# Optimization experiments

Measured on AMD Instinct MI355X. Metric: run time of the kernel, lower is better.

Reference implementation:

```python
import jax, jax.numpy as jnp
import numpy as np

N = 50000
E = 800000
IN_DIM = 128
HID_DIM = 128
OUT_DIM = 128
EPS = 1e-5


def setup_inputs() -> dict:
    key = jax.random.key(0)
    ks = jax.random.split(key, 6)
    x = jax.random.normal(ks[0], (N, IN_DIM), dtype=jnp.float32)
    src = jax.random.randint(ks[1], (E,), 0, N, dtype=jnp.int32)
    dst = jax.random.randint(ks[2], (E,), 0, N, dtype=jnp.int32)
    W1 = jax.random.normal(ks[3], (IN_DIM, HID_DIM), dtype=jnp.float32) / np.sqrt(IN_DIM)
    W2 = jax.random.normal(ks[4], (HID_DIM, OUT_DIM), dtype=jnp.float32) / np.sqrt(HID_DIM)
    return {
        "x": x, "src": src, "dst": dst,
        "W1": W1, "b1": jnp.zeros((HID_DIM,), jnp.float32),
        "gamma1": jnp.ones((HID_DIM,), jnp.float32), "beta1": jnp.zeros((HID_DIM,), jnp.float32),
        "W2": W2, "b2": jnp.zeros((OUT_DIM,), jnp.float32),
        "gamma2": jnp.ones((OUT_DIM,), jnp.float32), "beta2": jnp.zeros((OUT_DIM,), jnp.float32),
    }


def _degrees(src, dst, n):
    ones = jnp.ones(src.shape[0], jnp.float32)
    out_deg = jax.ops.segment_sum(ones, src, num_segments=n)
    in_deg = jax.ops.segment_sum(ones, dst, num_segments=n)
    # DGL norm='both' clamps degree to min 1 before pow(-0.5)
    return jnp.clip(out_deg, 1.0) ** -0.5, jnp.clip(in_deg, 1.0) ** -0.5


def _gconv(h, src, dst, d_out, d_in, W, b):
    h = h * d_out[:, None]                                   # [N, d] src-side norm
    m = jax.ops.segment_sum(h[src], dst, num_segments=h.shape[0])  # SpMM aggregate
    m = m * d_in[:, None]                                    # dst-side norm
    return m @ W + b


def _bn(h, gamma, beta):
    mu = jnp.mean(h, axis=0)
    var = jnp.var(h, axis=0)  # biased, matches torch BN training forward
    return gamma * (h - mu) * jax.lax.rsqrt(var + EPS) + beta


def reference(x, src, dst, W1, b1, gamma1, beta1, W2, b2, gamma2, beta2):
    d_out, d_in = _degrees(src, dst, x.shape[0])
    h1 = jax.nn.relu(_bn(_gconv(x, src, dst, d_out, d_in, W1, b1), gamma1, beta1))
    # dropout is identity in eval mode
    h2 = _bn(_gconv(h1, src, dst, d_out, d_in, W2, b2), gamma2, beta2)
    return jax.nn.relu(h2 + h1)
```

## Files before the change

### kernel.cpp

```cpp
#include <hip/hip_runtime.h>
#include <hip/hip_fp16.h>

#define NODES 50000
#define EDGES 800000
#define DIM 128
#define EPS_BN 1e-5f
#define SCAN_B 1024
#define SCAN_NB ((NODES + SCAN_B - 1) / SCAN_B)
#define GEMM_NB ((NODES + 63) / 64)
#define NCH 64
#define CHE (EDGES / NCH)
#define NR 4
#define RNG (NODES / NR)

typedef _Float16 half8 __attribute__((ext_vector_type(8)));
typedef float floatx4 __attribute__((ext_vector_type(4)));

union H8 { half8 v; __half2 h2[4]; };

__global__ __launch_bounds__(256) void hist_part_kernel(const int* __restrict__ src,
                                                        const int* __restrict__ dst,
                                                        unsigned short* __restrict__ Psrc,
                                                        unsigned short* __restrict__ Pdst) {
    __shared__ int h[RNG];
    int chunk = blockIdx.x & (NCH - 1);
    int range = blockIdx.x >> 6;
    const int* arr = blockIdx.y ? dst : src;
    unsigned short* P = blockIdx.y ? Pdst : Psrc;
    int base = range * RNG;
    for (int i = threadIdx.x; i < RNG; i += 256) h[i] = 0;
    __syncthreads();
    int e0 = chunk * CHE;
    for (int e = e0 + threadIdx.x; e < e0 + CHE; e += 256) {
        unsigned r = (unsigned)(arr[e] - base);
        if (r < (unsigned)RNG) atomicAdd(&h[r], 1);
    }
    __syncthreads();
    for (int i = threadIdx.x; i < RNG; i += 256)
        P[(size_t)chunk * NODES + base + i] = (unsigned short)h[i];
}

__global__ __launch_bounds__(256) void combine_kernel(const unsigned short* __restrict__ Psrc,
                                                      unsigned short* __restrict__ Pdst,
                                                      int* __restrict__ cnt_in,
                                                      float* __restrict__ dn_out,
                                                      float* __restrict__ dn_in) {
    int v = blockIdx.x * 256 + threadIdx.x;
    if (v >= NODES) return;
    int s = 0;
    #pragma unroll 8
    for (int j = 0; j < NCH; ++j) s += Psrc[(size_t)j * NODES + v];
    dn_out[v] = rsqrtf((float)max(s, 1));
    int run = 0;
    for (int j = 0; j < NCH; ++j) {
        int t = Pdst[(size_t)j * NODES + v];
        Pdst[(size_t)j * NODES + v] = (unsigned short)run;
        run += t;
    }
    cnt_in[v] = run;
    dn_in[v] = rsqrtf((float)max(run, 1));
}

__global__ __launch_bounds__(SCAN_B) void scan_p1_kernel(const int* __restrict__ cnt,
                                                         int* __restrict__ row_ptr,
                                                         int* __restrict__ blk_sums) {
    __shared__ int sm[SCAN_B];
    int t = threadIdx.x;
    int idx = blockIdx.x * SCAN_B + t;
    int v = (idx < NODES) ? cnt[idx] : 0;
    sm[t] = v;
    __syncthreads();
    #pragma unroll
    for (int off = 1; off < SCAN_B; off <<= 1) {
        int u = (t >= off) ? sm[t - off] : 0;
        __syncthreads();
        sm[t] += u;
        __syncthreads();
    }
    if (idx < NODES) row_ptr[idx] = sm[t] - v;
    if (t == SCAN_B - 1) blk_sums[blockIdx.x] = sm[t];
}

__global__ __launch_bounds__(SCAN_B) void scan_p3_kernel(int* __restrict__ row_ptr,
                                                         const int* __restrict__ blk_sums) {
    __shared__ int soff;
    int t = threadIdx.x;
    if (t < 64) {
        int v = (t < blockIdx.x) ? blk_sums[t] : 0;
        #pragma unroll
        for (int off = 32; off > 0; off >>= 1) v += __shfl_xor(v, off);
        if (t == 0) soff = v;
    }
    __syncthreads();
    int idx = blockIdx.x * SCAN_B + t;
    if (idx < NODES) row_ptr[idx] += soff;
    if (idx == 0) row_ptr[NODES] = EDGES;
}

__global__ __launch_bounds__(256) void fill_kernel(const int* __restrict__ src,
                                                   const int* __restrict__ dst,
                                                   const int* __restrict__ row_ptr,
                                                   const unsigned short* __restrict__ Pdst,
                                                   int* __restrict__ csr_src) {
    __shared__ int h[RNG];
    int chunk = blockIdx.x & (NCH - 1);
    int range = blockIdx.x >> 6;
    int base = range * RNG;
    for (int i = threadIdx.x; i < RNG; i += 256) h[i] = 0;
    __syncthreads();
    int e0 = chunk * CHE;
    const unsigned short* Pj = Pdst + (size_t)chunk * NODES;
    for (int e = e0 + threadIdx.x; e < e0 + CHE; e += 256) {
        int d = dst[e];
        unsigned r = (unsigned)(d - base);
        if (r < (unsigned)RNG) {
            int local = atomicAdd(&h[r], 1);
            csr_src[row_ptr[d] + (int)Pj[d] + local] = src[e];
        }
    }
}

__global__ __launch_bounds__(256) void w2h_kernel(const float* __restrict__ W1,
                                                  const float* __restrict__ W2,
                                                  __half* __restrict__ WhT1,
                                                  __half* __restrict__ WhT2) {
    int idx = blockIdx.x * 256 + threadIdx.x;
    const float* W = (idx < 16384) ? W1 : W2;
    __half* D = (idx < 16384) ? WhT1 : WhT2;
    int i = idx & 16383;
    int n = i >> 7;
    int k = i & 127;
    D[i] = __float2half(W[k * DIM + n]);
}

__global__ __launch_bounds__(256) void prescale_kernel(const float* __restrict__ x,
                                                       const float* __restrict__ dn_out,
                                                       __half* __restrict__ hs) {
    int idx = blockIdx.x * 256 + threadIdx.x;
    if (idx >= NODES * 16) return;
    int row = idx >> 4;
    int c8 = (idx & 15) * 8;
    float sc = dn_out[row];
    const float* xp = x + (size_t)row * DIM + c8;
    float4 v0 = *(const float4*)xp;
    float4 v1 = *(const float4*)(xp + 4);
    H8 u;
    u.h2[0] = __floats2half2_rn(v0.x * sc, v0.y * sc);
    u.h2[1] = __floats2half2_rn(v0.z * sc, v0.w * sc);
    u.h2[2] = __floats2half2_rn(v1.x * sc, v1.y * sc);
    u.h2[3] = __floats2half2_rn(v1.z * sc, v1.w * sc);
    *(half8*)((char*)hs + ((size_t)row * DIM + c8) * 2) = u.v;
}

__device__ __forceinline__ void acc_h8(half8 raw, float* a) {
    H8 u; u.v = raw;
    #pragma unroll
    for (int k = 0; k < 4; ++k) {
        float2 f = __half22float2(u.h2[k]);
        a[2 * k] += f.x;
        a[2 * k + 1] += f.y;
    }
}

__global__ __launch_bounds__(256) void pull_kernel(const __half* __restrict__ hs,
                                                   const int* __restrict__ row_ptr,
                                                   const int* __restrict__ csr_src,
                                                   const float* __restrict__ dn_in,
                                                   __half* __restrict__ agg) {
    int wid = threadIdx.x >> 6;
    int node = blockIdx.x * 4 + wid;
    if (node >= NODES) return;
    int lane = threadIdx.x & 63;
    int q = lane >> 4;
    int c = lane & 15;
    const char* base = (const char*)hs;
    int beg = row_ptr[node];
    int end = row_ptr[node + 1];
    float a[8];
    #pragma unroll
    for (int i = 0; i < 8; ++i) a[i] = 0.f;
    int eb = beg;
    for (; eb + 8 <= end; eb += 8) {
        int s0 = csr_src[eb + q];
        int s1 = csr_src[eb + 4 + q];
        half8 v0 = *(const half8*)(base + (size_t)s0 * 256 + c * 16);
        half8 v1 = *(const half8*)(base + (size_t)s1 * 256 + c * 16);
        acc_h8(v0, a);
        acc_h8(v1, a);
    }
    for (; eb + 4 <= end; eb += 4) {
        int s0 = csr_src[eb + q];
        half8 v0 = *(const half8*)(base + (size_t)s0 * 256 + c * 16);
        acc_h8(v0, a);
    }
    if (eb + q < end) {
        int s0 = csr_src[eb + q];
        half8 v0 = *(const half8*)(base + (size_t)s0 * 256 + c * 16);
        acc_h8(v0, a);
    }
    #pragma unroll
    for (int i = 0; i < 8; ++i) a[i] += __shfl_xor(a[i], 32);
    #pragma unroll
    for (int i = 0; i < 8; ++i) a[i] += __shfl_xor(a[i], 16);
    if (lane < 16) {
        float sc = dn_in[node];
        H8 u;
        #pragma unroll
        for (int k = 0; k < 4; ++k)
            u.h2[k] = __floats2half2_rn(a[2 * k] * sc, a[2 * k + 1] * sc);
        *(half8*)((char*)agg + (size_t)node * 256 + c * 16) = u.v;
    }
}

__global__ __launch_bounds__(256) void gemm_mfma_kernel(const __half* __restrict__ A,
                                                        const __half* __restrict__ WhT,
                                                        const float* __restrict__ bias,
                                                        __half* __restrict__ hraw,
                                                        float* __restrict__ partial) {
    __shared__ float smem[8704];
    __half* wl = (__half*)smem;

    int t = threadIdx.x;

    #pragma unroll
    for (int i = 0; i < 8; ++i) {
        int cch = t + 256 * i;
        int n = cch >> 4;
        int ch = cch & 15;
        *(float4*)((char*)wl + n * 272 + ch * 16) =
            *(const float4*)((const char*)WhT + n * 256 + ch * 16);
    }

    int w = t >> 6;
    int lane = t & 63;
    int m = lane & 15;
    int quad = lane >> 4;
    int r0 = blockIdx.x * 64 + w * 16;
    int arow = r0 + m;

    half8 afrag[4];
    if (arow < NODES) {
        const char* ap = (const char*)(A + (size_t)arow * DIM);
        #pragma unroll
        for (int kt = 0; kt < 4; ++kt)
            afrag[kt] = *(const half8*)(ap + kt * 64 + quad * 16);
    } else {
        #pragma unroll
        for (int kt = 0; kt < 4; ++kt)
            #pragma unroll
            for (int j = 0; j < 8; ++j)
                afrag[kt][j] = (_Float16)0.0f;
    }

    floatx4 acc[8];
    floatx4 zf = {0.f, 0.f, 0.f, 0.f};
    #pragma unroll
    for (int ct = 0; ct < 8; ++ct) acc[ct] = zf;

    __syncthreads();

    #pragma unroll
    for (int kt = 0; kt < 4; ++kt) {
        #pragma unroll
        for (int ct = 0; ct < 8; ++ct) {
            half8 b = *(const half8*)((const char*)wl + (ct * 16 + m) * 272 + kt * 64 + quad * 16);
            acc[ct] = __builtin_amdgcn_mfma_f32_16x16x32_f16(afrag[kt], b, acc[ct], 0, 0, 0);
        }
    }

    __syncthreads();

    float* ps = smem;
    int g = w * 4 + quad;
    #pragma unroll
    for (int ct = 0; ct < 8; ++ct) {
        int col = ct * 16 + m;
        float bb = bias[col];
        float cs = 0.f, cq = 0.f;
        #pragma unroll
        for (int reg = 0; reg < 4; ++reg) {
            int row = r0 + quad * 4 + reg;
            if (row < NODES) {
                float o = acc[ct][reg] + bb;
                hraw[(size_t)row * DIM + col] = __float2half(o);
                cs += o;
                cq += o * o;
            }
        }
        ps[g * 128 + col] = cs;
        ps[2048 + g * 128 + col] = cq;
    }
    __syncthreads();

    if (t < 128) {
        float s = 0.f;
        #pragma unroll
        for (int gg = 0; gg < 16; ++gg) s += ps[gg * 128 + t];
        partial[(size_t)blockIdx.x * 256 + t] = s;
    } else {
        int cc = t - 128;
        float s = 0.f;
        #pragma unroll
        for (int gg = 0; gg < 16; ++gg) s += ps[2048 + gg * 128 + cc];
        partial[(size_t)blockIdx.x * 256 + 128 + cc] = s;
    }
}

__global__ __launch_bounds__(256) void stats_s1_kernel(const float* __restrict__ partial,
                                                       float* __restrict__ p2) {
    int t = threadIdx.x;
    float s = 0.f;
    for (int b = blockIdx.x; b < GEMM_NB; b += 32) s += partial[(size_t)b * 256 + t];
    p2[blockIdx.x * 256 + t] = s;
}

__global__ __launch_bounds__(256) void stats_s2_kernel(const float* __restrict__ p2,
                                                       float* __restrict__ stats) {
    int t = threadIdx.x;
    float s = 0.f;
    #pragma unroll
    for (int b = 0; b < 32; ++b) s += p2[b * 256 + t];
    stats[t] = s;
}

__global__ __launch_bounds__(256) void bn_relu_scale_kernel(const __half* __restrict__ hraw,
                                                            __half* __restrict__ h1r,
                                                            __half* __restrict__ hs,
                                                            const float* __restrict__ stats,
                                                            const float* __restrict__ g,
                                                            const float* __restrict__ be,
                                                            const float* __restrict__ dn_out) {
    int idx = blockIdx.x * 256 + threadIdx.x;
    if (idx >= NODES * 16) return;
    int row = idx >> 4;
    int c8 = (idx & 15) * 8;
    const float invN = 1.0f / NODES;
    H8 u;
    u.v = *(const half8*)((const char*)hraw + ((size_t)row * DIM + c8) * 2);
    float o[8];
    #pragma unroll
    for (int k = 0; k < 4; ++k) {
        float2 f = __half22float2(u.h2[k]);
        o[2 * k] = f.x;
        o[2 * k + 1] = f.y;
    }
    #pragma unroll
    for (int j = 0; j < 8; ++j) {
        int cj = c8 + j;
        float mu = stats[cj] * invN;
        float var = stats[DIM + cj] * invN - mu * mu;
        float w = g[cj] * rsqrtf(var + EPS_BN);
        o[j] = fmaxf(w * (o[j] - mu) + be[cj], 0.f);
    }
    H8 ur, us;
    float sc = dn_out[row];
    #pragma unroll
    for (int k = 0; k < 4; ++k) {
        ur.h2[k] = __floats2half2_rn(o[2 * k], o[2 * k + 1]);
        us.h2[k] = __floats2half2_rn(o[2 * k] * sc, o[2 * k + 1] * sc);
    }
    *(half8*)((char*)h1r + ((size_t)row * DIM + c8) * 2) = ur.v;
    *(half8*)((char*)hs + ((size_t)row * DIM + c8) * 2) = us.v;
}

__global__ __launch_bounds__(256) void bn_res_relu_kernel(const __half* __restrict__ hraw,
                                                          const __half* __restrict__ h1r,
                                                          float* __restrict__ out,
                                                          const float* __restrict__ stats,
                                                          const float* __restrict__ g,
                                                          const float* __restrict__ be) {
    int idx = blockIdx.x * 256 + threadIdx.x;
    if (idx >= NODES * 16) return;
    int row = idx >> 4;
    int c8 = (idx & 15) * 8;
    const float invN = 1.0f / NODES;
    H8 u, ur;
    u.v = *(const half8*)((const char*)hraw + ((size_t)row * DIM + c8) * 2);
    ur.v = *(const half8*)((const char*)h1r + ((size_t)row * DIM + c8) * 2);
    float o[8], r[8];
    #pragma unroll
    for (int k = 0; k < 4; ++k) {
        float2 f = __half22float2(u.h2[k]);
        float2 fr = __half22float2(ur.h2[k]);
        o[2 * k] = f.x; o[2 * k + 1] = f.y;
        r[2 * k] = fr.x; r[2 * k + 1] = fr.y;
    }
    #pragma unroll
    for (int j = 0; j < 8; ++j) {
        int cj = c8 + j;
        float mu = stats[cj] * invN;
        float var = stats[DIM + cj] * invN - mu * mu;
        float w = g[cj] * rsqrtf(var + EPS_BN);
        o[j] = fmaxf(w * (o[j] - mu) + be[cj] + r[j], 0.f);
    }
    float* op = out + (size_t)row * DIM + c8;
    float4 o0 = {o[0], o[1], o[2], o[3]};
    float4 o1 = {o[4], o[5], o[6], o[7]};
    *(float4*)op = o0;
    *(float4*)(op + 4) = o1;
}

extern "C" void kernel_launch(void* const* d_in, const int* in_sizes, int n_in,
                              void* d_out, int out_size, void* d_ws, size_t ws_size,
                              hipStream_t stream) {
    const float* x      = (const float*)d_in[0];
    const int*   src    = (const int*)d_in[1];
    const int*   dst    = (const int*)d_in[2];
    const float* W1     = (const float*)d_in[3];
    const float* b1     = (const float*)d_in[4];
    const float* gamma1 = (const float*)d_in[5];
    const float* beta1  = (const float*)d_in[6];
    const float* W2     = (const float*)d_in[7];
    const float* b2     = (const float*)d_in[8];
    const float* gamma2 = (const float*)d_in[9];
    const float* beta2  = (const float*)d_in[10];
    float* out = (float*)d_out;
    __half* hs = (__half*)d_out;

    char* wsc = (char*)d_ws;
    int*   cnt_in   = (int*)wsc;                     wsc += NODES * 4;
    float* dn_out   = (float*)wsc;                   wsc += NODES * 4;
    float* dn_in    = (float*)wsc;                   wsc += NODES * 4;
    int*   row_ptr  = (int*)wsc;                     wsc += (NODES + 1) * 4;
    int*   csr_src  = (int*)wsc;                     wsc += EDGES * 4;
    float* stats    = (float*)wsc;                   wsc += 2 * DIM * 4;
    int*   blk_sums = (int*)wsc;                     wsc += 64 * 4;
    __half* WhT1    = (__half*)wsc;                  wsc += DIM * DIM * 2;
    __half* WhT2    = (__half*)wsc;                  wsc += DIM * DIM * 2;
    float* partial  = (float*)wsc;                   wsc += (size_t)GEMM_NB * 256 * 4;
    float* p2       = (float*)wsc;                   wsc += 32 * 256 * 4;
    unsigned short* Psrc = (unsigned short*)wsc;     wsc += (size_t)NCH * NODES * 2;
    unsigned short* Pdst = (unsigned short*)wsc;     wsc += (size_t)NCH * NODES * 2;
    __half* agg     = (__half*)wsc;                  wsc += (size_t)NODES * DIM * 2;
    __half* hraw    = (__half*)wsc;                  wsc += (size_t)NODES * DIM * 2;
    __half* h1r     = (__half*)wsc;                  wsc += (size_t)NODES * DIM * 2;

    const int T = 256;
    const int grid_pull = (NODES + 3) / 4;
    const int grid_e16  = (NODES * 16 + T - 1) / T;

    hist_part_kernel<<<dim3(NR * NCH, 2), T, 0, stream>>>(src, dst, Psrc, Pdst);
    combine_kernel<<<(NODES + T - 1) / T, T, 0, stream>>>(Psrc, Pdst, cnt_in, dn_out, dn_in);
    scan_p1_kernel<<<SCAN_NB, SCAN_B, 0, stream>>>(cnt_in, row_ptr, blk_sums);
    scan_p3_kernel<<<SCAN_NB, SCAN_B, 0, stream>>>(row_ptr, blk_sums);
    fill_kernel<<<NR * NCH, T, 0, stream>>>(src, dst, row_ptr, Pdst, csr_src);

    w2h_kernel<<<128, T, 0, stream>>>(W1, W2, WhT1, WhT2);

    prescale_kernel<<<grid_e16, T, 0, stream>>>(x, dn_out, hs);
    pull_kernel<<<grid_pull, T, 0, stream>>>(hs, row_ptr, csr_src, dn_in, agg);
    gemm_mfma_kernel<<<GEMM_NB, T, 0, stream>>>(agg, WhT1, b1, hraw, partial);
    stats_s1_kernel<<<32, T, 0, stream>>>(partial, p2);
    stats_s2_kernel<<<1, T, 0, stream>>>(p2, stats);
    bn_relu_scale_kernel<<<grid_e16, T, 0, stream>>>(hraw, h1r, hs, stats, gamma1, beta1, dn_out);

    pull_kernel<<<grid_pull, T, 0, stream>>>(hs, row_ptr, csr_src, dn_in, agg);
    gemm_mfma_kernel<<<GEMM_NB, T, 0, stream>>>(agg, WhT2, b2, hraw, partial);
    stats_s1_kernel<<<32, T, 0, stream>>>(partial, p2);
    stats_s2_kernel<<<1, T, 0, stream>>>(p2, stats);
    bn_res_relu_kernel<<<grid_e16, T, 0, stream>>>(hraw, h1r, out, stats, gamma2, beta2);
}
```

Before: 283.7 us.

## Fuse neighbor gather into MFMA GEMM, atomic BN stats, drop h1r buffer

Merges the CSR pull aggregation and the MFMA GEMM into one kernel. Each block gathers 64 aggregated rows into LDS and feeds them straight to the matrix multiply, so the fp16 agg buffer is never written to or read from global memory. The partial-sum buffer and the stats_s1 pass are replaced by float atomics into 32 slots. Those slots are zeroed by w2h and again by stats_s2. The separate h1r residual buffer is removed: the residual is rebuilt from the degree-scaled hs times sqrt(degree). This saves a store but may change fp16 rounding, and the fused kernel runs each wave serially over 16 nodes with much fewer blocks and heavier LDS use, which could cut latency hiding for the gather.

```diff
diff --git a/kernel.cpp b/kernel.cpp
--- a/kernel.cpp
+++ b/kernel.cpp
@@ -7,7 +7,7 @@
 #define EPS_BN 1e-5f
 #define SCAN_B 1024
 #define SCAN_NB ((NODES + SCAN_B - 1) / SCAN_B)
-#define GEMM_NB ((NODES + 63) / 64)
+#define PG_NB ((NODES + 63) / 64)
 #define NCH 64
 #define CHE (EDGES / NCH)
 #define NR 4
@@ -44,14 +44,18 @@
                                                       unsigned short* __restrict__ Pdst,
                                                       int* __restrict__ cnt_in,
                                                       float* __restrict__ dn_out,
+                                                      float* __restrict__ sdeg,
                                                       float* __restrict__ dn_in) {
     int v = blockIdx.x * 256 + threadIdx.x;
     if (v >= NODES) return;
     int s = 0;
     #pragma unroll 8
     for (int j = 0; j < NCH; ++j) s += Psrc[(size_t)j * NODES + v];
-    dn_out[v] = rsqrtf((float)max(s, 1));
+    float fs = (float)max(s, 1);
+    dn_out[v] = rsqrtf(fs);
+    sdeg[v] = sqrtf(fs);
     int run = 0;
+    #pragma unroll 8
     for (int j = 0; j < NCH; ++j) {
         int t = Pdst[(size_t)j * NODES + v];
         Pdst[(size_t)j * NODES + v] = (unsigned short)run;
@@ -123,8 +127,10 @@
 __global__ __launch_bounds__(256) void w2h_kernel(const float* __restrict__ W1,
                                                   const float* __restrict__ W2,
                                                   __half* __restrict__ WhT1,
-                                                  __half* __restrict__ WhT2) {
+                                                  __half* __restrict__ WhT2,
+                                                  float* __restrict__ p2) {
     int idx = blockIdx.x * 256 + threadIdx.x;
+    if (blockIdx.x < 32) p2[blockIdx.x * 256 + threadIdx.x] = 0.f;
     const float* W = (idx < 16384) ? W1 : W2;
     __half* D = (idx < 16384) ? WhT1 : WhT2;
     int i = idx & 16383;
@@ -162,63 +168,18 @@
     }
 }
 
-__global__ __launch_bounds__(256) void pull_kernel(const __half* __restrict__ hs,
-                                                   const int* __restrict__ row_ptr,
-                                                   const int* __restrict__ csr_src,
-                                                   const float* __restrict__ dn_in,
-                                                   __half* __restrict__ agg) {
-    int wid = threadIdx.x >> 6;
-    int node = blockIdx.x * 4 + wid;
-    if (node >= NODES) return;
-    int lane = threadIdx.x & 63;
-    int q = lane >> 4;
-    int c = lane & 15;
-    const char* base = (const char*)hs;
-    int beg = row_ptr[node];
-    int end = row_ptr[node + 1];
-    float a[8];
-    #pragma unroll
-    for (int i = 0; i < 8; ++i) a[i] = 0.f;
-    int eb = beg;
-    for (; eb + 8 <= end; eb += 8) {
-        int s0 = csr_src[eb + q];
-        int s1 = csr_src[eb + 4 + q];
-        half8 v0 = *(const half8*)(base + (size_t)s0 * 256 + c * 16);
-        half8 v1 = *(const half8*)(base + (size_t)s1 * 256 + c * 16);
-        acc_h8(v0, a);
-        acc_h8(v1, a);
-    }
-    for (; eb + 4 <= end; eb += 4) {
-        int s0 = csr_src[eb + q];
-        half8 v0 = *(const half8*)(base + (size_t)s0 * 256 + c * 16);
-        acc_h8(v0, a);
-    }
-    if (eb + q < end) {
-        int s0 = csr_src[eb + q];
-        half8 v0 = *(const half8*)(base + (size_t)s0 * 256 + c * 16);
-        acc_h8(v0, a);
-    }
-    #pragma unroll
-    for (int i = 0; i < 8; ++i) a[i] += __shfl_xor(a[i], 32);
-    #pragma unroll
-    for (int i = 0; i < 8; ++i) a[i] += __shfl_xor(a[i], 16);
-    if (lane < 16) {
-        float sc = dn_in[node];
-        H8 u;
-        #pragma unroll
-        for (int k = 0; k < 4; ++k)
-            u.h2[k] = __floats2half2_rn(a[2 * k] * sc, a[2 * k + 1] * sc);
-        *(half8*)((char*)agg + (size_t)node * 256 + c * 16) = u.v;
-    }
-}
-
-__global__ __launch_bounds__(256) void gemm_mfma_kernel(const __half* __restrict__ A,
-                                                        const __half* __restrict__ WhT,
-                                                        const float* __restrict__ bias,
-                                                        __half* __restrict__ hraw,
-                                                        float* __restrict__ partial) {
-    __shared__ float smem[8704];
+__global__ __launch_bounds__(256) void pullgemm_kernel(const __half* __restrict__ hs,
+                                                       const int* __restrict__ row_ptr,
+                                                       const int* __restrict__ csr_src,
+                                                       const float* __restrict__ dn_in,
+                                                       const __half* __restrict__ WhT,
+                                                       const float* __restrict__ bias,
+                                                       __half* __restrict__ hraw,
+                                                       float* __restrict__ p2) {
+    __shared__ float smem[13056];
     __half* wl = (__half*)smem;
+    char* at = (char*)smem + 34816;
+    float* ps = (float*)at;
 
     int t = threadIdx.x;
 
@@ -233,31 +194,71 @@
 
     int w = t >> 6;
     int lane = t & 63;
+    int q = lane >> 4;
+    int c = lane & 15;
+    int r0 = blockIdx.x * 64;
+    const char* base = (const char*)hs;
+
+    for (int i = 0; i < 16; ++i) {
+        int node = r0 + w * 16 + i;
+        char* arow = at + (w * 16 + i) * 272 + c * 16;
+        if (node < NODES) {
+            int beg = row_ptr[node];
+            int end = row_ptr[node + 1];
+            float a[8];
+            #pragma unroll
+            for (int k = 0; k < 8; ++k) a[k] = 0.f;
+            int eb = beg;
+            for (; eb + 8 <= end; eb += 8) {
+                int s0 = csr_src[eb + q];
+                int s1 = csr_src[eb + 4 + q];
+                half8 v0 = *(const half8*)(base + (size_t)s0 * 256 + c * 16);
+                half8 v1 = *(const half8*)(base + (size_t)s1 * 256 + c * 16);
+                acc_h8(v0, a);
+                acc_h8(v1, a);
+            }
+            for (; eb + 4 <= end; eb += 4) {
+                int s0 = csr_src[eb + q];
+                half8 v0 = *(const half8*)(base + (size_t)s0 * 256 + c * 16);
+                acc_h8(v0, a);
+            }
+            if (eb + q < end) {
+                int s0 = csr_src[eb + q];
+                half8 v0 = *(const half8*)(base + (size_t)s0 * 256 + c * 16);
+                acc_h8(v0, a);
+            }
+            #pragma unroll
+            for (int k = 0; k < 8; ++k) a[k] += __shfl_xor(a[k], 32);
+            #pragma unroll
+            for (int k = 0; k < 8; ++k) a[k] += __shfl_xor(a[k], 16);
+            if (lane < 16) {
+                float sc = dn_in[node];
+                H8 u;
+                #pragma unroll
+                for (int k = 0; k < 4; ++k)
+                    u.h2[k] = __floats2half2_rn(a[2 * k] * sc, a[2 * k + 1] * sc);
+                *(half8*)arow = u.v;
+            }
+        } else if (lane < 16) {
+            H8 z;
+            #pragma unroll
+            for (int k = 0; k < 4; ++k) z.h2[k] = __floats2half2_rn(0.f, 0.f);
+            *(half8*)arow = z.v;
+        }
+    }
+    __syncthreads();
+
     int m = lane & 15;
     int quad = lane >> 4;
-    int r0 = blockIdx.x * 64 + w * 16;
-    int arow = r0 + m;
-
     half8 afrag[4];
-    if (arow < NODES) {
-        const char* ap = (const char*)(A + (size_t)arow * DIM);
-        #pragma unroll
-        for (int kt = 0; kt < 4; ++kt)
-            afrag[kt] = *(const half8*)(ap + kt * 64 + quad * 16);
-    } else {
-        #pragma unroll
-        for (int kt = 0; kt < 4; ++kt)
-            #pragma unroll
-            for (int j = 0; j < 8; ++j)
-                afrag[kt][j] = (_Float16)0.0f;
-    }
+    #pragma unroll
+    for (int kt = 0; kt < 4; ++kt)
+        afrag[kt] = *(const half8*)(at + (w * 16 + m) * 272 + kt * 64 + quad * 16);
 
     floatx4 acc[8];
     floatx4 zf = {0.f, 0.f, 0.f, 0.f};
     #pragma unroll
     for (int ct = 0; ct < 8; ++ct) acc[ct] = zf;
-
-    __syncthreads();
 
     #pragma unroll
     for (int kt = 0; kt < 4; ++kt) {
@@ -267,10 +268,9 @@
             acc[ct] = __builtin_amdgcn_mfma_f32_16x16x32_f16(afrag[kt], b, acc[ct], 0, 0, 0);
         }
     }
-
-    __syncthreads();
-
-    float* ps = smem;
+    __syncthreads();
+
+    int rr0 = r0 + w * 16;
     int g = w * 4 + quad;
     #pragma unroll
     for (int ct = 0; ct < 8; ++ct) {
@@ -279,7 +279,7 @@
         float cs = 0.f, cq = 0.f;
         #pragma unroll
         for (int reg = 0; reg < 4; ++reg) {
-            int row = r0 + quad * 4 + reg;
+            int row = rr0 + quad * 4 + reg;
             if (row < NODES) {
                 float o = acc[ct][reg] + bb;
                 hraw[(size_t)row * DIM + col] = __float2half(o);
@@ -292,39 +292,33 @@
     }
     __syncthreads();
 
+    float* pslot = p2 + (blockIdx.x & 31) * 256;
     if (t < 128) {
         float s = 0.f;
         #pragma unroll
         for (int gg = 0; gg < 16; ++gg) s += ps[gg * 128 + t];
-        partial[(size_t)blockIdx.x * 256 + t] = s;
+        atomicAdd(pslot + t, s);
     } else {
         int cc = t - 128;
         float s = 0.f;
         #pragma unroll
         for (int gg = 0; gg < 16; ++gg) s += ps[2048 + gg * 128 + cc];
-        partial[(size_t)blockIdx.x * 256 + 128 + cc] = s;
-    }
-}
-
-__global__ __launch_bounds__(256) void stats_s1_kernel(const float* __restrict__ partial,
-                                                       float* __restrict__ p2) {
-    int t = threadIdx.x;
-    float s = 0.f;
-    for (int b = blockIdx.x; b < GEMM_NB; b += 32) s += partial[(size_t)b * 256 + t];
-    p2[blockIdx.x * 256 + t] = s;
-}
-
-__global__ __launch_bounds__(256) void stats_s2_kernel(const float* __restrict__ p2,
+        atomicAdd(pslot + 128 + cc, s);
+    }
+}
+
+__global__ __launch_bounds__(256) void stats_s2_kernel(float* __restrict__ p2,
                                                        float* __restrict__ stats) {
     int t = threadIdx.x;
     float s = 0.f;
     #pragma unroll
     for (int b = 0; b < 32; ++b) s += p2[b * 256 + t];
     stats[t] = s;
+    #pragma unroll
+    for (int b = 0; b < 32; ++b) p2[b * 256 + t] = 0.f;
 }
 
 __global__ __launch_bounds__(256) void bn_relu_scale_kernel(const __half* __restrict__ hraw,
-                                                            __half* __restrict__ h1r,
                                                             __half* __restrict__ hs,
                                                             const float* __restrict__ stats,
                                                             const float* __restrict__ g,
@@ -352,19 +346,17 @@
         float w = g[cj] * rsqrtf(var + EPS_BN);
         o[j] = fmaxf(w * (o[j] - mu) + be[cj], 0.f);
     }
-    H8 ur, us;
+    H8 us;
     float sc = dn_out[row];
     #pragma unroll
-    for (int k = 0; k < 4; ++k) {
-        ur.h2[k] = __floats2half2_rn(o[2 * k], o[2 * k + 1]);
+    for (int k = 0; k < 4; ++k)
         us.h2[k] = __floats2half2_rn(o[2 * k] * sc, o[2 * k + 1] * sc);
-    }
-    *(half8*)((char*)h1r + ((size_t)row * DIM + c8) * 2) = ur.v;
     *(half8*)((char*)hs + ((size_t)row * DIM + c8) * 2) = us.v;
 }
 
 __global__ __launch_bounds__(256) void bn_res_relu_kernel(const __half* __restrict__ hraw,
-                                                          const __half* __restrict__ h1r,
+                                                          const __half* __restrict__ hs,
+                                                          const float* __restrict__ sdeg,
                                                           float* __restrict__ out,
                                                           const float* __restrict__ stats,
                                                           const float* __restrict__ g,
@@ -374,16 +366,17 @@
     int row = idx >> 4;
     int c8 = (idx & 15) * 8;
     const float invN = 1.0f / NODES;
+    float sd = sdeg[row];
     H8 u, ur;
     u.v = *(const half8*)((const char*)hraw + ((size_t)row * DIM + c8) * 2);
-    ur.v = *(const half8*)((const char*)h1r + ((size_t)row * DIM + c8) * 2);
+    ur.v = *(const half8*)((const char*)hs + ((size_t)row * DIM + c8) * 2);
     float o[8], r[8];
     #pragma unroll
     for (int k = 0; k < 4; ++k) {
         float2 f = __half22float2(u.h2[k]);
         float2 fr = __half22float2(ur.h2[k]);
         o[2 * k] = f.x; o[2 * k + 1] = f.y;
-        r[2 * k] = fr.x; r[2 * k + 1] = fr.y;
+        r[2 * k] = fr.x * sd; r[2 * k + 1] = fr.y * sd;
     }
     #pragma unroll
     for (int j = 0; j < 8; ++j) {
@@ -415,11 +408,11 @@
     const float* gamma2 = (const float*)d_in[9];
     const float* beta2  = (const float*)d_in[10];
     float* out = (float*)d_out;
-    __half* hs = (__half*)d_out;
 
     char* wsc = (char*)d_ws;
     int*   cnt_in   = (int*)wsc;                     wsc += NODES * 4;
     float* dn_out   = (float*)wsc;                   wsc += NODES * 4;
+    float* sdeg     = (float*)wsc;                   wsc += NODES * 4;
     float* dn_in    = (float*)wsc;                   wsc += NODES * 4;
     int*   row_ptr  = (int*)wsc;                     wsc += (NODES + 1) * 4;
     int*   csr_src  = (int*)wsc;                     wsc += EDGES * 4;
@@ -427,36 +420,29 @@
     int*   blk_sums = (int*)wsc;                     wsc += 64 * 4;
     __half* WhT1    = (__half*)wsc;                  wsc += DIM * DIM * 2;
     __half* WhT2    = (__half*)wsc;                  wsc += DIM * DIM * 2;
-    float* partial  = (float*)wsc;                   wsc += (size_t)GEMM_NB * 256 * 4;
     float* p2       = (float*)wsc;                   wsc += 32 * 256 * 4;
     unsigned short* Psrc = (unsigned short*)wsc;     wsc += (size_t)NCH * NODES * 2;
     unsigned short* Pdst = (unsigned short*)wsc;     wsc += (size_t)NCH * NODES * 2;
-    __half* agg     = (__half*)wsc;                  wsc += (size_t)NODES * DIM * 2;
+    __half* hs      = (__half*)wsc;                  wsc += (size_t)NODES * DIM * 2;
     __half* hraw    = (__half*)wsc;                  wsc += (size_t)NODES * DIM * 2;
-    __half* h1r     = (__half*)wsc;                  wsc += (size_t)NODES * DIM * 2;
 
     const int T = 256;
-    const int grid_pull = (NODES + 3) / 4;
-    const int grid_e16  = (NODES * 16 + T - 1) / T;
+    const int grid_e16 = (NODES * 16 + T - 1) / T;
 
     hist_part_kernel<<<dim3(NR * NCH, 2), T, 0, stream>>>(src, dst, Psrc, Pdst);
-    combine_kernel<<<(NODES + T - 1) / T, T, 0, stream>>>(Psrc, Pdst, cnt_in, dn_out, dn_in);
+    combine_kernel<<<(NODES + T - 1) / T, T, 0, stream>>>(Psrc, Pdst, cnt_in, dn_out, sdeg, dn_in);
     scan_p1_kernel<<<SCAN_NB, SCAN_B, 0, stream>>>(cnt_in, row_ptr, blk_sums);
     scan_p3_kernel<<<SCAN_NB, SCAN_B, 0, stream>>>(row_ptr, blk_sums);
     fill_kernel<<<NR * NCH, T, 0, stream>>>(src, dst, row_ptr, Pdst, csr_src);
 
-    w2h_kernel<<<128, T, 0, stream>>>(W1, W2, WhT1, WhT2);
+    w2h_kernel<<<128, T, 0, stream>>>(W1, W2, WhT1, WhT2, p2);
 
     prescale_kernel<<<grid_e16, T, 0, stream>>>(x, dn_out, hs);
-    pull_kernel<<<grid_pull, T, 0, stream>>>(hs, row_ptr, csr_src, dn_in, agg);
-    gemm_mfma_kernel<<<GEMM_NB, T, 0, stream>>>(agg, WhT1, b1, hraw, partial);
-    stats_s1_kernel<<<32, T, 0, stream>>>(partial, p2);
+    pullgemm_kernel<<<PG_NB, T, 0, stream>>>(hs, row_ptr, csr_src, dn_in, WhT1, b1, hraw, p2);
     stats_s2_kernel<<<1, T, 0, stream>>>(p2, stats);
-    bn_relu_scale_kernel<<<grid_e16, T, 0, stream>>>(hraw, h1r, hs, stats, gamma1, beta1, dn_out);
-
-    pull_kernel<<<grid_pull, T, 0, stream>>>(hs, row_ptr, csr_src, dn_in, agg);
-    gemm_mfma_kernel<<<GEMM_NB, T, 0, stream>>>(agg, WhT2, b2, hraw, partial);
-    stats_s1_kernel<<<32, T, 0, stream>>>(partial, p2);
+    bn_relu_scale_kernel<<<grid_e16, T, 0, stream>>>(hraw, hs, stats, gamma1, beta1, dn_out);
+
+    pullgemm_kernel<<<PG_NB, T, 0, stream>>>(hs, row_ptr, csr_src, dn_in, WhT2, b2, hraw, p2);
     stats_s2_kernel<<<1, T, 0, stream>>>(p2, stats);
-    bn_res_relu_kernel<<<grid_e16, T, 0, stream>>>(hraw, h1r, out, stats, gamma2, beta2);
-}
+    bn_res_relu_kernel<<<grid_e16, T, 0, stream>>>(hraw, hs, sdeg, out, stats, gamma2, beta2);
+}
```

New measurement: 380.5 us. +34.1%, slower.
